# Kernel tuning notes

Measured on AMD Instinct MI355X. Metric: run time of the kernel, lower is better.

## Reference

```python
import jax, jax.numpy as jnp
import numpy as np

V, H, L, NH, I, P = 50257, 768, 12, 12, 3072, 2048
B, S = 2, 1024
HD = H // NH
MASK_VALUE = -1e9  # fp32 path in the torch code


def layer_norm(x, w, b, eps=1e-5):
    m = jnp.mean(x, axis=-1, keepdims=True)
    v = jnp.mean((x - m) ** 2, axis=-1, keepdims=True)
    return (x - m) / jnp.sqrt(v + eps) * w + b


def setup_inputs() -> dict:
    key = jax.random.key(0)
    ks = iter(jax.random.split(key, 16))
    std = 0.02
    nrm = lambda k, shape: jax.random.normal(k, shape, jnp.float32) * std
    inp = {
        "input_ids": jax.random.randint(next(ks), (B, S), 0, V),
        "attention_mask": jnp.ones((B, S), jnp.int32),
        "tok_emb": nrm(next(ks), (V, H)),
        "pos_emb": nrm(next(ks), (P, H)),
        "ln1_w": jnp.ones((L, H)), "ln1_b": jnp.zeros((L, H)),
        "qw": nrm(next(ks), (L, H, H)),
        "kw": nrm(next(ks), (L, H, H)),
        "vw": nrm(next(ks), (L, H, H)),
        "ow": nrm(next(ks), (L, H, H)), "ob": jnp.zeros((L, H)),
        "ln2_w": jnp.ones((L, H)), "ln2_b": jnp.zeros((L, H)),
        "w1": nrm(next(ks), (L, I, H)), "b1": jnp.zeros((L, I)),
        "w2": nrm(next(ks), (L, H, I)), "b2": jnp.zeros((L, H)),
        "lnf_w": jnp.ones((H,)), "lnf_b": jnp.zeros((H,)),
        "lm_head_w": nrm(next(ks), (V, H)),
    }
    return inp


def reference(input_ids, attention_mask, tok_emb, pos_emb, ln1_w, ln1_b, qw, kw, vw,
              ow, ob, ln2_w, ln2_b, w1, b1, w2, b2, lnf_w, lnf_b, lm_head_w):
    scale = 1.0 / np.sqrt(HD)
    # embeddings
    x = tok_emb[input_ids] + pos_emb[jnp.arange(S)][None]  # [B,S,H]
    causal = jnp.tril(jnp.ones((S, S), bool))              # [S,S]
    pad = attention_mask.astype(bool)[:, None, None, :]    # [B,1,1,S]
    mask = causal[None, None] & pad                        # [B,1,S,S]

    def block(x, p):
        l1w, l1b, qw_, kw_, vw_, ow_, ob_, l2w, l2b, w1_, b1_, w2_, b2_ = p
        h = layer_norm(x, l1w, l1b)
        q = (h @ qw_.T).reshape(B, S, NH, HD).transpose(0, 2, 1, 3)  # [B,NH,S,HD]
        k = (h @ kw_.T).reshape(B, S, NH, HD).transpose(0, 2, 1, 3)
        v = (h @ vw_.T).reshape(B, S, NH, HD).transpose(0, 2, 1, 3)
        scores = jnp.einsum('bhqd,bhkd->bhqk', q, k) * scale
        scores = jnp.where(mask, scores, MASK_VALUE)
        attn = jax.nn.softmax(scores, axis=-1)
        a = jnp.einsum('bhqk,bhkd->bhqd', attn, v)
        a = a.transpose(0, 2, 1, 3).reshape(B, S, H)
        x = x + a @ ow_.T + ob_
        h2 = layer_norm(x, l2w, l2b)
        ff = jax.nn.gelu(h2 @ w1_.T + b1_, approximate=False) @ w2_.T + b2_
        return x + ff, None

    x, _ = jax.lax.scan(block, x, (ln1_w, ln1_b, qw, kw, vw, ow, ob,
                                   ln2_w, ln2_b, w1, b1, w2, b2))
    h = layer_norm(x, lnf_w, lnf_b)
    logits = h @ lm_head_w.T  # [B,S,V]
    return logits
```

## Files before the change

### kernel.cpp

```cpp
#include <hip/hip_runtime.h>
#include <hip/hip_bf16.h>
#include <cmath>

typedef unsigned short u16;
typedef __bf16 bf16_t;
typedef __bf16 bf16x8 __attribute__((ext_vector_type(8)));
typedef float f32x4 __attribute__((ext_vector_type(4)));

#define HDIM   768
#define NHEAD  12
#define HD     64
#define SEQ    1024
#define BATCH  2
#define NLAYER 12
#define FFI    3072
#define VOCAB  50257
#define NTOK   (BATCH*SEQ)
#define QKVW   2304

__device__ inline u16 f2bf(float f) {
  bf16_t h = (bf16_t)f;
  return __builtin_bit_cast(u16, h);
}

__device__ __forceinline__ void gl_lds16(const u16* g, u16* l) {
  __builtin_amdgcn_global_load_lds(
      (const __attribute__((address_space(1))) unsigned int*)g,
      (__attribute__((address_space(3))) unsigned int*)l, 16, 0, 0);
}

#define BKK 64

template<typename WT, typename OT, int EPI, int TMt, int TNt>
__global__ __launch_bounds__(256, 2) void gemm_nt(
    const u16* __restrict__ A, const WT* __restrict__ W, OT* __restrict__ C,
    const float* __restrict__ bias,
    int M, int N, int K, int lda, int ldb, int ldc,
    long long aOut, long long aIn, long long bOut, long long bIn,
    long long cOut, long long cIn, int zdiv, int causal, int ksplit, int swz)
{
  constexpr int WMt = TMt / 2, WNt = TNt / 2;
  constexpr int MI = WMt / 16, NJ = WNt / 16;
  constexpr int ACH = TMt / 32;
  constexpr int BCH = TNt / 32;

  __shared__ __align__(16) u16 sA[TMt * BKK];
  __shared__ __align__(16) u16 sB[TNt * BKK];

  int bx = blockIdx.x, by = blockIdx.y;
  if (swz) {
    int id = blockIdx.x;
    int xcd = id & 7, j = id >> 3;
    bx = j & 15;
    by = xcd * 50 + (j >> 4);
    if (by >= 393) return;
  }

  int z = blockIdx.z;
  if (zdiv > 1) {
    int zo = z / zdiv, zi = z - zo * zdiv;
    A += zo * aOut + zi * aIn;
    W += zo * bOut + zi * bIn;
    C += zo * cOut + zi * cIn;
  }
  int kt0 = 0, kend = K;
  if (ksplit > 1) {
    int kc = K / ksplit;
    kt0 = z * kc;
    kend = kt0 + kc;
  }
  int mt = bx * TMt;
  int nt = by * TNt;
  if (causal && nt > mt + (TMt - 1)) return;

  int t = threadIdx.x;
  int w = t >> 6, l = t & 63;
  int wm = (w >> 1) * WMt, wn = (w & 1) * WNt;
  int quad = l >> 4, mr = l & 15;

  int lrow = l >> 3;
  int lcol = (l & 7) * 8;

  int arow = t >> 3, akc = (t & 7) * 8;

  f32x4 acc[MI][NJ] = {};

  for (int kt = kt0; kt < kend; kt += BKK) {
    #pragma unroll
    for (int i = 0; i < ACH; i++) {
      int row = w * (TMt / 4) + i * 8;
      gl_lds16(A + (size_t)(mt + row + lrow) * lda + kt + lcol, &sA[row * BKK]);
    }
    if constexpr (sizeof(WT) == 2) {
      #pragma unroll
      for (int i = 0; i < BCH; i++) {
        int row = w * (TNt / 4) + i * 8;
        int gr = nt + row + lrow; if (gr >= N) gr = N - 1;
        gl_lds16((const u16*)W + (size_t)gr * ldb + kt + lcol, &sB[row * BKK]);
      }
    } else {
      #pragma unroll
      for (int i = 0; i < BCH; i++) {
        int row = arow + i * 32;
        int gr = nt + row; if (gr >= N) gr = N - 1;
        const float* src = (const float*)W + (size_t)gr * ldb + kt + akc;
        float4 f0 = *(const float4*)(src);
        float4 f1 = *(const float4*)(src + 4);
        uint4 p;
        p.x = (unsigned)f2bf(f0.x) | ((unsigned)f2bf(f0.y) << 16);
        p.y = (unsigned)f2bf(f0.z) | ((unsigned)f2bf(f0.w) << 16);
        p.z = (unsigned)f2bf(f1.x) | ((unsigned)f2bf(f1.y) << 16);
        p.w = (unsigned)f2bf(f1.z) | ((unsigned)f2bf(f1.w) << 16);
        *(uint4*)(&sB[row * BKK + akc]) = p;
      }
    }
    __syncthreads();
    #pragma unroll
    for (int kk = 0; kk < BKK; kk += 32) {
      bf16x8 af[MI], bfr[NJ];
      #pragma unroll
      for (int i = 0; i < MI; i++)
        af[i] = *(const bf16x8*)(&sA[(wm + i * 16 + mr) * BKK + kk + quad * 8]);
      #pragma unroll
      for (int j = 0; j < NJ; j++)
        bfr[j] = *(const bf16x8*)(&sB[(wn + j * 16 + mr) * BKK + kk + quad * 8]);
      #pragma unroll
      for (int i = 0; i < MI; i++)
        #pragma unroll
        for (int j = 0; j < NJ; j++)
          acc[i][j] = __builtin_amdgcn_mfma_f32_16x16x32_bf16(af[i], bfr[j], acc[i][j], 0, 0, 0);
    }
    __syncthreads();
  }

  #pragma unroll
  for (int i = 0; i < MI; i++)
    #pragma unroll
    for (int j = 0; j < NJ; j++)
      #pragma unroll
      for (int r = 0; r < 4; r++) {
        int gm = mt + wm + i * 16 + quad * 4 + r;
        int gn = nt + wn + j * 16 + mr;
        if (gn < N) {
          float v = acc[i][j][r];
          size_t idx = (size_t)gm * ldc + gn;
          if constexpr (EPI == 3) {
            float add = v + (kt0 == 0 ? bias[gn] : 0.0f);
            atomicAdd(&((float*)C)[idx], add);
          } else if constexpr (EPI == 2) {
            float u = v + bias[gn];
            float g = 0.5f * u * (1.0f + erff(u * 0.70710678118654752f));
            C[idx] = (OT)f2bf(g);
          } else {
            if constexpr (sizeof(OT) == 2) C[idx] = f2bf(v);
            else                           C[idx] = v;
          }
        }
      }
}

__global__ __launch_bounds__(256) void cvt_w(
    const float* __restrict__ src, u16* __restrict__ dst,
    long long srcLs, long long dstLs, long long perL, long long total)
{
  long long i8 = ((long long)blockIdx.x * 256 + threadIdx.x) * 8;
  if (i8 >= total) return;
  long long l = i8 / perL;
  long long r = i8 - l * perL;
  const float4* s4 = (const float4*)(src + l * srcLs + r);
  float4 f0 = s4[0], f1 = s4[1];
  uint4 p;
  p.x = (unsigned)f2bf(f0.x) | ((unsigned)f2bf(f0.y) << 16);
  p.y = (unsigned)f2bf(f0.z) | ((unsigned)f2bf(f0.w) << 16);
  p.z = (unsigned)f2bf(f1.x) | ((unsigned)f2bf(f1.y) << 16);
  p.w = (unsigned)f2bf(f1.z) | ((unsigned)f2bf(f1.w) << 16);
  *(uint4*)(dst + l * dstLs + r) = p;
}

__global__ __launch_bounds__(256) void ln_bf16(
    const float* __restrict__ x, const float* __restrict__ w,
    const float* __restrict__ b, u16* __restrict__ out)
{
  __shared__ float redA[4], redB[4];
  int row = blockIdx.x;
  const float* xr = x + (size_t)row * HDIM;
  int t = threadIdx.x;
  float v0 = xr[t], v1 = xr[t + 256], v2 = xr[t + 512];
  float s  = v0 + v1 + v2;
  float s2 = v0 * v0 + v1 * v1 + v2 * v2;
  #pragma unroll
  for (int o = 32; o > 0; o >>= 1) { s += __shfl_xor(s, o); s2 += __shfl_xor(s2, o); }
  if ((t & 63) == 0) { redA[t >> 6] = s; redB[t >> 6] = s2; }
  __syncthreads();
  float S  = redA[0] + redA[1] + redA[2] + redA[3];
  float S2 = redB[0] + redB[1] + redB[2] + redB[3];
  float mean = S * (1.0f / HDIM);
  float var  = S2 * (1.0f / HDIM) - mean * mean;
  float rstd = rsqrtf(var + 1e-5f);
  u16* orow = out + (size_t)row * HDIM;
  orow[t]       = f2bf((v0 - mean) * rstd * w[t]       + b[t]);
  orow[t + 256] = f2bf((v1 - mean) * rstd * w[t + 256] + b[t + 256]);
  orow[t + 512] = f2bf((v2 - mean) * rstd * w[t + 512] + b[t + 512]);
}

__global__ __launch_bounds__(256) void softmax_causal(
    const u16* __restrict__ scores, u16* __restrict__ P,
    const int* __restrict__ amask)
{
  __shared__ float red[4];
  int row = blockIdx.x;
  int z  = row >> 10;
  int qi = row & (SEQ - 1);
  int b  = z / NHEAD;
  const u16* s = scores + (size_t)row * SEQ;
  u16* p = P + (size_t)row * SEQ;
  int t = threadIdx.x;
  int j0 = t * 4;
  ushort4 sv = *(const ushort4*)(s + j0);
  int4    mv = *(const int4*)(amask + b * SEQ + j0);
  u16 sa[4] = {sv.x, sv.y, sv.z, sv.w};
  int ma[4] = {mv.x, mv.y, mv.z, mv.w};
  float vals[4];
  float mx = -3.4e38f;
  #pragma unroll
  for (int i = 0; i < 4; i++) {
    float v = -1e9f;
    if (j0 + i <= qi && ma[i] != 0)
      v = (float)__builtin_bit_cast(bf16_t, sa[i]) * 0.125f;
    vals[i] = v;
    mx = fmaxf(mx, v);
  }
  #pragma unroll
  for (int o = 32; o > 0; o >>= 1) mx = fmaxf(mx, __shfl_xor(mx, o));
  if ((t & 63) == 0) red[t >> 6] = mx;
  __syncthreads();
  mx = fmaxf(fmaxf(red[0], red[1]), fmaxf(red[2], red[3]));
  float e[4]; float sum = 0.0f;
  #pragma unroll
  for (int i = 0; i < 4; i++) { e[i] = expf(vals[i] - mx); sum += e[i]; }
  #pragma unroll
  for (int o = 32; o > 0; o >>= 1) sum += __shfl_xor(sum, o);
  __syncthreads();
  if ((t & 63) == 0) red[t >> 6] = sum;
  __syncthreads();
  float inv = 1.0f / (red[0] + red[1] + red[2] + red[3]);
  ushort4 ov;
  ov.x = f2bf(e[0] * inv); ov.y = f2bf(e[1] * inv);
  ov.z = f2bf(e[2] * inv); ov.w = f2bf(e[3] * inv);
  *(ushort4*)(p + j0) = ov;
}

__global__ void embed_k(const int* __restrict__ ids, const float* __restrict__ tok,
                        const float* __restrict__ pos, float* __restrict__ x)
{
  int tkn = blockIdx.x;
  int sidx = tkn & (SEQ - 1);
  int id = ids[tkn];
  int t = threadIdx.x;
  float4 a = ((const float4*)tok)[(size_t)id * 192 + t];
  float4 b = ((const float4*)pos)[(size_t)sidx * 192 + t];
  float4 o = {a.x + b.x, a.y + b.y, a.z + b.z, a.w + b.w};
  ((float4*)x)[(size_t)tkn * 192 + t] = o;
}

__global__ __launch_bounds__(256) void transpose_v(const u16* __restrict__ qkv, u16* __restrict__ vT)
{
  __shared__ u16 tile[64][68];
  int z = blockIdx.y;
  int s0 = blockIdx.x * 64;
  int b = z / NHEAD, hh = z - b * NHEAD;
  const u16* src = qkv + (size_t)(b * SEQ + s0) * QKVW + 1536 + hh * HD;
  int t = threadIdx.x;
  int c4 = (t & 15) * 4, r0 = t >> 4;
  #pragma unroll
  for (int i = 0; i < 4; i++) {
    int row = r0 + i * 16;
    *(uint2*)(&tile[row][c4]) = *(const uint2*)(src + (size_t)row * QKVW + c4);
  }
  __syncthreads();
  u16* dst = vT + (size_t)z * HD * SEQ + s0;
  #pragma unroll
  for (int i = 0; i < 4; i++) {
    int d = r0 + i * 16;
    ushort4 o;
    o.x = tile[c4 + 0][d];
    o.y = tile[c4 + 1][d];
    o.z = tile[c4 + 2][d];
    o.w = tile[c4 + 3][d];
    *(ushort4*)(dst + (size_t)d * SEQ + c4) = o;
  }
}

extern "C" void kernel_launch(void* const* d_in, const int* in_sizes, int n_in,
                              void* d_out, int out_size, void* d_ws, size_t ws_size,
                              hipStream_t stream)
{
  const int*   ids   = (const int*)d_in[0];
  const int*   amask = (const int*)d_in[1];
  const float* tok   = (const float*)d_in[2];
  const float* pos   = (const float*)d_in[3];
  const float* ln1w  = (const float*)d_in[4];
  const float* ln1b  = (const float*)d_in[5];
  const float* qw    = (const float*)d_in[6];
  const float* kw    = (const float*)d_in[7];
  const float* vw    = (const float*)d_in[8];
  const float* ow    = (const float*)d_in[9];
  const float* ob    = (const float*)d_in[10];
  const float* ln2w  = (const float*)d_in[11];
  const float* ln2b  = (const float*)d_in[12];
  const float* w1    = (const float*)d_in[13];
  const float* b1    = (const float*)d_in[14];
  const float* w2    = (const float*)d_in[15];
  const float* b2    = (const float*)d_in[16];
  const float* lnfw  = (const float*)d_in[17];
  const float* lnfb  = (const float*)d_in[18];
  const float* lmw   = (const float*)d_in[19];

  char* ws = (char*)d_ws;
  float* x    = (float*)(ws);
  u16*   h    = (u16*)  (ws + 6291456);
  u16*   qkv  = (u16*)  (ws + 9437184);
  u16*   vT   = (u16*)  (ws + 18874368);
  u16*   ab   = (u16*)  (ws + 22020096);
  u16*   ffb  = (u16*)  (ws + 25165824);
  u16*   wlm  = (u16*)  (ws + 37748736);
  bool lmbf = ws_size >= (size_t)114943488;

  u16* scores = (u16*)d_out;
  u16* Pm     = (u16*)((char*)d_out + 50331648);
  u16* wqkv   = (u16*)((char*)d_out + 100663296);
  u16* wob    = wqkv + (size_t)NLAYER * QKVW * HDIM;
  u16* w1b    = wob  + (size_t)NLAYER * HDIM * HDIM;
  u16* w2b    = w1b  + (size_t)NLAYER * FFI  * HDIM;

  cvt_w<<<3456,  256, 0, stream>>>(qw, wqkv,           589824, 1769472, 589824, 7077888LL);
  cvt_w<<<3456,  256, 0, stream>>>(kw, wqkv + 589824,  589824, 1769472, 589824, 7077888LL);
  cvt_w<<<3456,  256, 0, stream>>>(vw, wqkv + 1179648, 589824, 1769472, 589824, 7077888LL);
  cvt_w<<<3456,  256, 0, stream>>>(ow, wob,            589824, 589824,  589824, 7077888LL);
  cvt_w<<<13824, 256, 0, stream>>>(w1, w1b,            2359296, 2359296, 2359296, 28311552LL);
  cvt_w<<<13824, 256, 0, stream>>>(w2, w2b,            2359296, 2359296, 2359296, 28311552LL);
  if (lmbf)
    cvt_w<<<18847, 256, 0, stream>>>(lmw, wlm, 0, 0, 38597376LL, 38597376LL);

  embed_k<<<NTOK, 192, 0, stream>>>(ids, tok, pos, x);

  for (int l = 0; l < NLAYER; l++) {
    ln_bf16<<<NTOK, 256, 0, stream>>>(x, ln1w + l * HDIM, ln1b + l * HDIM, h);

    gemm_nt<u16, u16, 0, 128, 128><<<dim3(16, 18), 256, 0, stream>>>(
        h, wqkv + (size_t)l * QKVW * HDIM, qkv, nullptr,
        NTOK, QKVW, HDIM, HDIM, HDIM, QKVW, 0, 0, 0, 0, 0, 0, 1, 0, 1, 0);

    transpose_v<<<dim3(16, BATCH * NHEAD), 256, 0, stream>>>(qkv, vT);

    gemm_nt<u16, u16, 0, 128, 128><<<dim3(8, 8, BATCH * NHEAD), 256, 0, stream>>>(
        qkv, qkv + 768, scores, nullptr,
        SEQ, SEQ, HD, QKVW, QKVW, SEQ,
        (long long)SEQ * QKVW, HD, (long long)SEQ * QKVW, HD,
        (long long)NHEAD * SEQ * SEQ, (long long)SEQ * SEQ, NHEAD, 1, 1, 0);

    softmax_causal<<<BATCH * NHEAD * SEQ, 256, 0, stream>>>(scores, Pm, amask);

    gemm_nt<u16, u16, 0, 64, 64><<<dim3(16, 1, BATCH * NHEAD), 256, 0, stream>>>(
        Pm, vT, ab, nullptr,
        SEQ, HD, SEQ, SEQ, SEQ, HDIM,
        (long long)NHEAD * SEQ * SEQ, (long long)SEQ * SEQ,
        (long long)NHEAD * HD * SEQ, (long long)HD * SEQ,
        (long long)SEQ * HDIM, HD, NHEAD, 0, 1, 0);

    gemm_nt<u16, float, 3, 128, 128><<<dim3(16, 6, 2), 256, 0, stream>>>(
        ab, wob + (size_t)l * HDIM * HDIM, x, ob + l * HDIM,
        NTOK, HDIM, HDIM, HDIM, HDIM, HDIM, 0, 0, 0, 0, 0, 0, 1, 0, 2, 0);

    ln_bf16<<<NTOK, 256, 0, stream>>>(x, ln2w + l * HDIM, ln2b + l * HDIM, h);

    gemm_nt<u16, u16, 2, 128, 128><<<dim3(16, 24), 256, 0, stream>>>(
        h, w1b + (size_t)l * FFI * HDIM, ffb, b1 + l * FFI,
        NTOK, FFI, HDIM, HDIM, HDIM, FFI, 0, 0, 0, 0, 0, 0, 1, 0, 1, 0);

    gemm_nt<u16, float, 3, 128, 128><<<dim3(16, 6, 4), 256, 0, stream>>>(
        ffb, w2b + (size_t)l * HDIM * FFI, x, b2 + l * HDIM,
        NTOK, HDIM, FFI, FFI, FFI, HDIM, 0, 0, 0, 0, 0, 0, 1, 0, 4, 0);
  }

  ln_bf16<<<NTOK, 256, 0, stream>>>(x, lnfw, lnfb, h);
  if (lmbf) {
    gemm_nt<u16, float, 0, 128, 128><<<6400, 256, 0, stream>>>(
        h, wlm, (float*)d_out, nullptr,
        NTOK, VOCAB, HDIM, HDIM, HDIM, VOCAB, 0, 0, 0, 0, 0, 0, 1, 0, 1, 1);
  } else {
    gemm_nt<float, float, 0, 128, 128><<<6400, 256, 0, stream>>>(
        h, lmw, (float*)d_out, nullptr,
        NTOK, VOCAB, HDIM, HDIM, HDIM, VOCAB, 0, 0, 0, 0, 0, 0, 1, 0, 1, 1);
  }
}
```

Measured before the change: 3.428 ms.

## Replace unfused attention pipeline with a fused causal flash-attention kernel

Swaps the V transpose, QK^T GEMM, row softmax and PV GEMM for one flash-attention kernel using an online softmax. It tiles 64 queries against 64-key blocks in shared memory, transposes V in LDS, skips key tiles above the causal diagonal and writes straight into the attention output buffer. This removes the full score and probability matrices from global memory, several launches, and the wasted upper-triangle work. In exchange the grid is small (384 blocks), per-block work is unbalanced along the diagonal, and each tile has several syncthreads.

```diff
diff --git a/kernel.cpp b/kernel.cpp
--- a/kernel.cpp
+++ b/kernel.cpp
@@ -157,6 +157,147 @@
           }
         }
       }
+}
+
+__global__ __launch_bounds__(256, 2) void flash_attn(
+    const u16* __restrict__ qkv, u16* __restrict__ ab, const int* __restrict__ amask)
+{
+  __shared__ __align__(16) u16 sQ[64 * 64];
+  __shared__ __align__(16) u16 sK[64 * 64];
+  __shared__ __align__(16) u16 sVT[64 * 72];
+  __shared__ __align__(16) u16 sPV[64 * 68];
+  __shared__ u16 s_am[SEQ];
+
+  int MT = blockIdx.x * 64;
+  int z  = blockIdx.y;
+  int b  = z / NHEAD, h = z - b * NHEAD;
+  const u16* qbase = qkv + (size_t)(b * SEQ) * QKVW + h * HD;
+  const u16* kbase = qbase + 768;
+  const u16* vbase = qbase + 1536;
+
+  int t = threadIdx.x;
+  int w = t >> 6, l = t & 63;
+  int quad = l >> 4, mr = l & 15;
+  int lrow = l >> 3, lcol = (l & 7) * 8;
+  int wm = w * 16;
+  int c4 = (t & 15) * 4, r0 = t >> 4;
+
+  #pragma unroll
+  for (int i = 0; i < 2; i++) {
+    int row = w * 16 + i * 8;
+    gl_lds16(qbase + (size_t)(MT + row + lrow) * QKVW + lcol, &sQ[row * 64]);
+  }
+  {
+    int4 mv = *(const int4*)(amask + b * SEQ + t * 4);
+    s_am[t * 4 + 0] = (u16)(mv.x != 0);
+    s_am[t * 4 + 1] = (u16)(mv.y != 0);
+    s_am[t * 4 + 2] = (u16)(mv.z != 0);
+    s_am[t * 4 + 3] = (u16)(mv.w != 0);
+  }
+
+  f32x4 oacc[4] = {};
+  float mrun[4] = {-3.0e38f, -3.0e38f, -3.0e38f, -3.0e38f};
+  float lrun[4] = {};
+
+  for (int jt = 0; jt <= MT; jt += 64) {
+    #pragma unroll
+    for (int i = 0; i < 2; i++) {
+      int row = w * 16 + i * 8;
+      gl_lds16(kbase + (size_t)(jt + row + lrow) * QKVW + lcol, &sK[row * 64]);
+    }
+    uint2 vr[4];
+    #pragma unroll
+    for (int i = 0; i < 4; i++)
+      vr[i] = *(const uint2*)(vbase + (size_t)(jt + r0 + i * 16) * QKVW + c4);
+    __syncthreads();
+    #pragma unroll
+    for (int i = 0; i < 4; i++)
+      *(uint2*)(&sPV[(r0 + i * 16) * 68 + c4]) = vr[i];
+    __syncthreads();
+    f32x4 sacc[4] = {};
+    #pragma unroll
+    for (int kk = 0; kk < 64; kk += 32) {
+      bf16x8 af = *(const bf16x8*)(&sQ[(wm + mr) * 64 + kk + quad * 8]);
+      #pragma unroll
+      for (int j = 0; j < 4; j++) {
+        bf16x8 bf = *(const bf16x8*)(&sK[(j * 16 + mr) * 64 + kk + quad * 8]);
+        sacc[j] = __builtin_amdgcn_mfma_f32_16x16x32_bf16(af, bf, sacc[j], 0, 0, 0);
+      }
+    }
+    #pragma unroll
+    for (int i = 0; i < 4; i++) {
+      int d = r0 + i * 16;
+      ushort4 o;
+      o.x = sPV[(c4 + 0) * 68 + d];
+      o.y = sPV[(c4 + 1) * 68 + d];
+      o.z = sPV[(c4 + 2) * 68 + d];
+      o.w = sPV[(c4 + 3) * 68 + d];
+      *(ushort4*)(&sVT[d * 72 + c4]) = o;
+    }
+    __syncthreads();
+    float sv[4][4];
+    float mx[4] = {-3.0e38f, -3.0e38f, -3.0e38f, -3.0e38f};
+    #pragma unroll
+    for (int j = 0; j < 4; j++) {
+      int colg = jt + j * 16 + mr;
+      bool am = s_am[colg] != 0;
+      #pragma unroll
+      for (int r = 0; r < 4; r++) {
+        int rowg = MT + wm + quad * 4 + r;
+        float v = (am && colg <= rowg) ? sacc[j][r] * 0.125f : -1e9f;
+        sv[j][r] = v;
+        mx[r] = fmaxf(mx[r], v);
+      }
+    }
+    #pragma unroll
+    for (int off = 8; off > 0; off >>= 1)
+      #pragma unroll
+      for (int r = 0; r < 4; r++) mx[r] = fmaxf(mx[r], __shfl_xor(mx[r], off));
+    float alpha[4], lsum[4];
+    #pragma unroll
+    for (int r = 0; r < 4; r++) {
+      float mn = fmaxf(mrun[r], mx[r]);
+      alpha[r] = expf(mrun[r] - mn);
+      mrun[r] = mn;
+      lsum[r] = 0.0f;
+    }
+    #pragma unroll
+    for (int j = 0; j < 4; j++)
+      #pragma unroll
+      for (int r = 0; r < 4; r++) {
+        float p = expf(sv[j][r] - mrun[r]);
+        lsum[r] += p;
+        sPV[(wm + quad * 4 + r) * 64 + j * 16 + mr] = f2bf(p);
+      }
+    #pragma unroll
+    for (int off = 8; off > 0; off >>= 1)
+      #pragma unroll
+      for (int r = 0; r < 4; r++) lsum[r] += __shfl_xor(lsum[r], off);
+    #pragma unroll
+    for (int r = 0; r < 4; r++) {
+      lrun[r] = lrun[r] * alpha[r] + lsum[r];
+      #pragma unroll
+      for (int j = 0; j < 4; j++) oacc[j][r] *= alpha[r];
+    }
+    #pragma unroll
+    for (int kk = 0; kk < 64; kk += 32) {
+      bf16x8 af = *(const bf16x8*)(&sPV[(wm + mr) * 64 + kk + quad * 8]);
+      #pragma unroll
+      for (int j = 0; j < 4; j++) {
+        bf16x8 bf = *(const bf16x8*)(&sVT[(j * 16 + mr) * 72 + kk + quad * 8]);
+        oacc[j] = __builtin_amdgcn_mfma_f32_16x16x32_bf16(af, bf, oacc[j], 0, 0, 0);
+      }
+    }
+  }
+  u16* orow = ab + (size_t)(b * SEQ + MT) * HDIM + h * HD;
+  #pragma unroll
+  for (int r = 0; r < 4; r++) {
+    float inv = 1.0f / lrun[r];
+    int rowl = wm + quad * 4 + r;
+    #pragma unroll
+    for (int j = 0; j < 4; j++)
+      orow[(size_t)rowl * HDIM + j * 16 + mr] = f2bf(oacc[j][r] * inv);
+  }
 }
 
 __global__ __launch_bounds__(256) void cvt_w(
@@ -203,53 +344,6 @@
   orow[t + 512] = f2bf((v2 - mean) * rstd * w[t + 512] + b[t + 512]);
 }
 
-__global__ __launch_bounds__(256) void softmax_causal(
-    const u16* __restrict__ scores, u16* __restrict__ P,
-    const int* __restrict__ amask)
-{
-  __shared__ float red[4];
-  int row = blockIdx.x;
-  int z  = row >> 10;
-  int qi = row & (SEQ - 1);
-  int b  = z / NHEAD;
-  const u16* s = scores + (size_t)row * SEQ;
-  u16* p = P + (size_t)row * SEQ;
-  int t = threadIdx.x;
-  int j0 = t * 4;
-  ushort4 sv = *(const ushort4*)(s + j0);
-  int4    mv = *(const int4*)(amask + b * SEQ + j0);
-  u16 sa[4] = {sv.x, sv.y, sv.z, sv.w};
-  int ma[4] = {mv.x, mv.y, mv.z, mv.w};
-  float vals[4];
-  float mx = -3.4e38f;
-  #pragma unroll
-  for (int i = 0; i < 4; i++) {
-    float v = -1e9f;
-    if (j0 + i <= qi && ma[i] != 0)
-      v = (float)__builtin_bit_cast(bf16_t, sa[i]) * 0.125f;
-    vals[i] = v;
-    mx = fmaxf(mx, v);
-  }
-  #pragma unroll
-  for (int o = 32; o > 0; o >>= 1) mx = fmaxf(mx, __shfl_xor(mx, o));
-  if ((t & 63) == 0) red[t >> 6] = mx;
-  __syncthreads();
-  mx = fmaxf(fmaxf(red[0], red[1]), fmaxf(red[2], red[3]));
-  float e[4]; float sum = 0.0f;
-  #pragma unroll
-  for (int i = 0; i < 4; i++) { e[i] = expf(vals[i] - mx); sum += e[i]; }
-  #pragma unroll
-  for (int o = 32; o > 0; o >>= 1) sum += __shfl_xor(sum, o);
-  __syncthreads();
-  if ((t & 63) == 0) red[t >> 6] = sum;
-  __syncthreads();
-  float inv = 1.0f / (red[0] + red[1] + red[2] + red[3]);
-  ushort4 ov;
-  ov.x = f2bf(e[0] * inv); ov.y = f2bf(e[1] * inv);
-  ov.z = f2bf(e[2] * inv); ov.w = f2bf(e[3] * inv);
-  *(ushort4*)(p + j0) = ov;
-}
-
 __global__ void embed_k(const int* __restrict__ ids, const float* __restrict__ tok,
                         const float* __restrict__ pos, float* __restrict__ x)
 {
@@ -261,34 +355,6 @@
   float4 b = ((const float4*)pos)[(size_t)sidx * 192 + t];
   float4 o = {a.x + b.x, a.y + b.y, a.z + b.z, a.w + b.w};
   ((float4*)x)[(size_t)tkn * 192 + t] = o;
-}
-
-__global__ __launch_bounds__(256) void transpose_v(const u16* __restrict__ qkv, u16* __restrict__ vT)
-{
-  __shared__ u16 tile[64][68];
-  int z = blockIdx.y;
-  int s0 = blockIdx.x * 64;
-  int b = z / NHEAD, hh = z - b * NHEAD;
-  const u16* src = qkv + (size_t)(b * SEQ + s0) * QKVW + 1536 + hh * HD;
-  int t = threadIdx.x;
-  int c4 = (t & 15) * 4, r0 = t >> 4;
-  #pragma unroll
-  for (int i = 0; i < 4; i++) {
-    int row = r0 + i * 16;
-    *(uint2*)(&tile[row][c4]) = *(const uint2*)(src + (size_t)row * QKVW + c4);
-  }
-  __syncthreads();
-  u16* dst = vT + (size_t)z * HD * SEQ + s0;
-  #pragma unroll
-  for (int i = 0; i < 4; i++) {
-    int d = r0 + i * 16;
-    ushort4 o;
-    o.x = tile[c4 + 0][d];
-    o.y = tile[c4 + 1][d];
-    o.z = tile[c4 + 2][d];
-    o.w = tile[c4 + 3][d];
-    *(ushort4*)(dst + (size_t)d * SEQ + c4) = o;
-  }
 }
 
 extern "C" void kernel_launch(void* const* d_in, const int* in_sizes, int n_in,
@@ -320,14 +386,11 @@
   float* x    = (float*)(ws);
   u16*   h    = (u16*)  (ws + 6291456);
   u16*   qkv  = (u16*)  (ws + 9437184);
-  u16*   vT   = (u16*)  (ws + 18874368);
   u16*   ab   = (u16*)  (ws + 22020096);
   u16*   ffb  = (u16*)  (ws + 25165824);
   u16*   wlm  = (u16*)  (ws + 37748736);
   bool lmbf = ws_size >= (size_t)114943488;
 
-  u16* scores = (u16*)d_out;
-  u16* Pm     = (u16*)((char*)d_out + 50331648);
   u16* wqkv   = (u16*)((char*)d_out + 100663296);
   u16* wob    = wqkv + (size_t)NLAYER * QKVW * HDIM;
   u16* w1b    = wob  + (size_t)NLAYER * HDIM * HDIM;
@@ -351,22 +414,7 @@
         h, wqkv + (size_t)l * QKVW * HDIM, qkv, nullptr,
         NTOK, QKVW, HDIM, HDIM, HDIM, QKVW, 0, 0, 0, 0, 0, 0, 1, 0, 1, 0);
 
-    transpose_v<<<dim3(16, BATCH * NHEAD), 256, 0, stream>>>(qkv, vT);
-
-    gemm_nt<u16, u16, 0, 128, 128><<<dim3(8, 8, BATCH * NHEAD), 256, 0, stream>>>(
-        qkv, qkv + 768, scores, nullptr,
-        SEQ, SEQ, HD, QKVW, QKVW, SEQ,
-        (long long)SEQ * QKVW, HD, (long long)SEQ * QKVW, HD,
-        (long long)NHEAD * SEQ * SEQ, (long long)SEQ * SEQ, NHEAD, 1, 1, 0);
-
-    softmax_causal<<<BATCH * NHEAD * SEQ, 256, 0, stream>>>(scores, Pm, amask);
-
-    gemm_nt<u16, u16, 0, 64, 64><<<dim3(16, 1, BATCH * NHEAD), 256, 0, stream>>>(
-        Pm, vT, ab, nullptr,
-        SEQ, HD, SEQ, SEQ, SEQ, HDIM,
-        (long long)NHEAD * SEQ * SEQ, (long long)SEQ * SEQ,
-        (long long)NHEAD * HD * SEQ, (long long)HD * SEQ,
-        (long long)SEQ * HDIM, HD, NHEAD, 0, 1, 0);
+    flash_attn<<<dim3(SEQ / 64, BATCH * NHEAD), 256, 0, stream>>>(qkv, ab, amask);
 
     gemm_nt<u16, float, 3, 128, 128><<<dim3(16, 6, 2), 256, 0, stream>>>(
         ab, wob + (size_t)l * HDIM * HDIM, x, ob + l * HDIM,
```

After: 3.424 ms. About the same (-0.1%).
